# Performance work log

Hardware: AMD Instinct MI355X
Metric: run time of the kernel (lower is better)

## Reference

```python
import jax, jax.numpy as jnp
import numpy as np

E = 300   # embedding_dim
H = 300   # lstm hidden per direction
V = 200000
S = 128   # number of sentences
L = 128   # max sentence length
D = 2 * H # bilstm output dim == attention model_dim
NEG = -1e30


def setup_inputs() -> dict:
    key = jax.random.key(0)
    ks = jax.random.split(key, 12)
    sd = 0.05
    return {
        "tokens": jax.random.randint(ks[0], (S, L), 0, V, dtype=jnp.int32),
        "lengths": jax.random.randint(ks[1], (S,), 1, L + 1, dtype=jnp.int32),
        "table": jax.random.normal(ks[2], (V, E), jnp.float32) * sd,
        "Wih_f": jax.random.normal(ks[3], (4 * H, E), jnp.float32) * sd,
        "Whh_f": jax.random.normal(ks[4], (4 * H, H), jnp.float32) * sd,
        "bih_f": jax.random.normal(ks[5], (4 * H,), jnp.float32) * sd,
        "bhh_f": jax.random.normal(ks[6], (4 * H,), jnp.float32) * sd,
        "Wih_b": jax.random.normal(ks[7], (4 * H, E), jnp.float32) * sd,
        "Whh_b": jax.random.normal(ks[8], (4 * H, H), jnp.float32) * sd,
        "bih_b": jax.random.normal(ks[9], (4 * H,), jnp.float32) * sd,
        "bhh_b": jax.random.normal(ks[10], (4 * H,), jnp.float32) * sd,
    }


def _lstm_dir(x, Wih, Whh, bih, bhh, reverse):
    # x: [N, E] -> hs: [N, H]; PyTorch gate order (i, f, g, o)
    xw = x @ Wih.T + (bih + bhh)  # hoist input projection out of the scan

    def step(carry, xt):
        h, c = carry
        g = xt + h @ Whh.T
        i, f, gg, o = jnp.split(g, 4, axis=-1)
        c = jax.nn.sigmoid(f) * c + jax.nn.sigmoid(i) * jnp.tanh(gg)
        h = jax.nn.sigmoid(o) * jnp.tanh(c)
        return (h, c), h

    init = (jnp.zeros((H,), x.dtype), jnp.zeros((H,), x.dtype))
    _, hs = jax.lax.scan(step, init, xw, reverse=reverse)
    return hs


def reference(tokens, lengths, table, Wih_f, Whh_f, bih_f, bhh_f,
              Wih_b, Whh_b, bih_b, bhh_b):
    lens = np.asarray(lengths)                       # concrete lengths (static)
    rows = np.repeat(np.arange(S), lens)             # [N] sentence id per token
    cols = np.concatenate([np.arange(int(l)) for l in lens])  # [N] pos in sentence

    flat_ids = tokens[rows, cols]                    # ragged concat of all sentences, [N]
    embeds = table[flat_ids]                         # [N, E]

    # single BiLSTM pass over the whole concatenated token stream (batch=1)
    h_fwd = _lstm_dir(embeds, Wih_f, Whh_f, bih_f, bhh_f, reverse=False)
    h_bwd = _lstm_dir(embeds, Wih_b, Whh_b, bih_b, bhh_b, reverse=True)
    lstm_out = jnp.concatenate([h_fwd, h_bwd], axis=-1)  # [N, D]

    # scatter back to padded [S, L, D] so per-sentence attention is batched
    padded = jnp.zeros((S, L, D), lstm_out.dtype).at[rows, cols].set(lstm_out)
    mask = jnp.asarray(np.arange(L)[None, :] < lens[:, None])  # [S, L]

    # per-sentence scaled dot-product self-attention (Q=K=V=lstm_out slice)
    scores = jnp.einsum('sqd,skd->sqk', padded, padded) / jnp.sqrt(jnp.float32(D))
    scores = jnp.where(mask[:, None, :], scores, NEG)  # key padding mask
    attn = jax.nn.softmax(scores, axis=-1)
    ctx = jnp.einsum('sqk,skd->sqd', attn, padded)     # [S, L, D]

    # max-pool over valid positions of each sentence
    ctx = jnp.where(mask[:, :, None], ctx, NEG)
    return jnp.max(ctx, axis=1)                        # [S, D]
```

## Files before the change

kernel.cpp:

```cpp
#include <hip/hip_runtime.h>
#include <stdint.h>

#define S_ 128
#define L_ 128
#define E_ 300
#define H_ 300
#define NMAX (S_*L_)
#define R_ 1200
#define D_ 600
#define XW_STRIDE ((size_t)NMAX*R_)

__global__ void prep_kernel(const int* __restrict__ lengths, int* __restrict__ meta,
                            int* __restrict__ map, unsigned long long* __restrict__ hbuf) {
    __shared__ int offs[S_];
    int tid = threadIdx.x;
    if (tid == 0) {
        int acc = 0;
        for (int s = 0; s < S_; s++) { offs[s] = acc; acc += lengths[s]; }
        meta[0] = acc;
    }
    __syncthreads();
    for (int s = tid; s < S_; s += blockDim.x) {
        int o = offs[s], len = lengths[s];
        for (int l = 0; l < len; l++) map[o + l] = s * L_ + l;
    }
    for (int i = tid; i < 2*2*320; i += blockDim.x) hbuf[i] = 0ull;
}

__global__ __launch_bounds__(256, 1) void xw_kernel(
    const int* __restrict__ tokens, const float* __restrict__ table,
    const float* __restrict__ Wih_f, const float* __restrict__ bih_f, const float* __restrict__ bhh_f,
    const float* __restrict__ Wih_b, const float* __restrict__ bih_b, const float* __restrict__ bhh_b,
    const int* __restrict__ meta, const int* __restrict__ map, float* __restrict__ xw) {
    const int N = meta[0];
    const int n0 = blockIdx.x * 32;
    if (n0 >= N) return;
    const int r = blockIdx.y * 256 + threadIdx.x;
    const bool vr = (r < 2*R_);
    const int dir = (r >= R_) ? 1 : 0;
    const int rr = r - dir * R_;
    const float* W = dir ? Wih_b : Wih_f;
    float bias = 0.f;
    float4 w4[75];
    if (vr) {
        bias = dir ? (bih_b[rr] + bhh_b[rr]) : (bih_f[rr] + bhh_f[rr]);
        #pragma unroll
        for (int j = 0; j < 75; j++) w4[j] = *(const float4*)(W + (size_t)rr * E_ + 4*j);
    } else {
        #pragma unroll
        for (int j = 0; j < 75; j++) w4[j] = make_float4(0.f, 0.f, 0.f, 0.f);
    }
    float* xwd = xw + (size_t)dir * XW_STRIDE;
    const int iend = min(32, N - n0);
    for (int i = 0; i < iend; i++) {
        const int n = n0 + i;
        const int tok = tokens[map[n]];
        const float* arow = table + (size_t)tok * E_;
        float a0 = bias, a1 = 0.f, a2 = 0.f, a3 = 0.f;
        #pragma unroll
        for (int j = 0; j < 75; j++) {
            float4 a4 = *(const float4*)(arow + 4*j);
            a0 = fmaf(w4[j].x, a4.x, a0);
            a1 = fmaf(w4[j].y, a4.y, a1);
            a2 = fmaf(w4[j].z, a4.z, a2);
            a3 = fmaf(w4[j].w, a4.w, a3);
        }
        if (vr) xwd[(size_t)n * R_ + rr] = (a0 + a1) + (a2 + a3);
    }
}

__device__ __forceinline__ float sel4(int m, float a, float b, float c, float d) {
    float r = a;
    r = (m == 1) ? b : r;
    r = (m == 2) ? c : r;
    r = (m == 3) ? d : r;
    return r;
}
__device__ __forceinline__ float sigm(float x) {
    return __builtin_amdgcn_rcpf(1.f + __expf(-x));
}
__device__ __forceinline__ float tanh_fast(float x) {
    return 1.f - 2.f * __builtin_amdgcn_rcpf(1.f + __expf(2.f * x));
}

__global__ __launch_bounds__(256, 1) void scan_kernel(
    const float* __restrict__ Whh_f, const float* __restrict__ Whh_b,
    const int* __restrict__ meta, const int* __restrict__ map,
    unsigned long long* __restrict__ hbuf, const float* __restrict__ xw,
    float* __restrict__ padded) {
    const int N = meta[0];
    const int b = blockIdx.x;
    const int dir = b / 10;
    const int blk = b % 10;
    const int tid = threadIdx.x;
    const int wave = tid >> 6;
    const int lane = tid & 63;
    const int pair = tid >> 1;
    const int half = tid & 1;
    const int gate = pair & 3;
    const int d = 30 * blk + (pair >> 2);
    const bool vd = (pair < 120);

    __shared__ float w_lds[120][300];
    __shared__ float hl[4][300];

    const float* Whh = dir ? Whh_b : Whh_f;
    for (int i = tid; i < 120 * 75; i += 256) {
        const int lr = i / 75;
        const int c4 = (i % 75) * 4;
        const int grow = (lr & 3) * H_ + blk * 30 + (lr >> 2);
        *(float4*)(&w_lds[lr][c4]) = *(const float4*)(Whh + (size_t)grow * H_ + c4);
    }
    __syncthreads();

    const int row = gate * H_ + (vd ? d : 0);
    const int cbase = half ? 152 : 0;
    const float* wrow = vd ? &w_lds[pair][cbase] : &w_lds[0][cbase];

    const float* xwd = xw + (size_t)dir * XW_STRIDE;
    unsigned long long* hb = hbuf + dir * 2 * 320;
    float* hw = hl[wave];

    float c = 0.f;
    const bool storer = (vd && gate == 0 && half == 0);
    const int pd = dir * H_ + d;

    for (int t = 0; t < N; t++) {
        const int n = dir ? (N - 1 - t) : t;
        const float xw_t = vd ? xwd[(size_t)n * R_ + row] : 0.f;
        const int   m_t  = map[n];

        const unsigned long long* hp = hb + (size_t)(t & 1) * 320;
        const unsigned int want = (unsigned int)t;
        unsigned long long v0, v1, v2, v3, v4;
        for (;;) {
            v0 = __hip_atomic_load(hp + lane,        __ATOMIC_RELAXED, __HIP_MEMORY_SCOPE_AGENT);
            v1 = __hip_atomic_load(hp + 64  + lane,  __ATOMIC_RELAXED, __HIP_MEMORY_SCOPE_AGENT);
            v2 = __hip_atomic_load(hp + 128 + lane,  __ATOMIC_RELAXED, __HIP_MEMORY_SCOPE_AGENT);
            v3 = __hip_atomic_load(hp + 192 + lane,  __ATOMIC_RELAXED, __HIP_MEMORY_SCOPE_AGENT);
            v4 = (lane < 44) ? __hip_atomic_load(hp + 256 + lane, __ATOMIC_RELAXED, __HIP_MEMORY_SCOPE_AGENT)
                             : ((unsigned long long)want << 32);
            bool ok = ((unsigned int)(v0 >> 32) == want) &&
                      ((unsigned int)(v1 >> 32) == want) &&
                      ((unsigned int)(v2 >> 32) == want) &&
                      ((unsigned int)(v3 >> 32) == want) &&
                      ((unsigned int)(v4 >> 32) == want);
            if (ok) break;
        }
        hw[lane]        = __uint_as_float((unsigned int)v0);
        hw[64  + lane]  = __uint_as_float((unsigned int)v1);
        hw[128 + lane]  = __uint_as_float((unsigned int)v2);
        hw[192 + lane]  = __uint_as_float((unsigned int)v3);
        if (lane < 44) hw[256 + lane] = __uint_as_float((unsigned int)v4);

        const float* hbase = hw + cbase;
        float a0 = 0.f, a1 = 0.f, a2 = 0.f, a3 = 0.f;
        #pragma unroll
        for (int j = 0; j < 37; j++) {
            const float4 wj = *(const float4*)(wrow + 4*j);
            const float4 h4 = *(const float4*)(hbase + 4*j);
            a0 = fmaf(wj.x, h4.x, a0);
            a1 = fmaf(wj.y, h4.y, a1);
            a2 = fmaf(wj.z, h4.z, a2);
            a3 = fmaf(wj.w, h4.w, a3);
        }
        if (half == 0) {
            const float4 wj = *(const float4*)(wrow + 148);
            const float4 h4 = *(const float4*)(hbase + 148);
            a0 = fmaf(wj.x, h4.x, a0);
            a1 = fmaf(wj.y, h4.y, a1);
            a2 = fmaf(wj.z, h4.z, a2);
            a3 = fmaf(wj.w, h4.w, a3);
        }
        float sum = (a0 + a1) + (a2 + a3);
        sum += __shfl_xor(sum, 1);
        const float acc = xw_t + sum;

        const float aa = acc;
        const float bb = __shfl_xor(acc, 2);
        const float cc = __shfl_xor(acc, 4);
        const float dd = __shfl_xor(bb, 4);
        const float vi = sel4(gate,     aa, bb, cc, dd);
        const float vf = sel4(gate ^ 1, aa, bb, cc, dd);
        const float vg = sel4(gate ^ 2, aa, bb, cc, dd);
        const float vo = sel4(gate ^ 3, aa, bb, cc, dd);

        c = sigm(vf) * c + sigm(vi) * tanh_fast(vg);
        const float h = sigm(vo) * tanh_fast(c);

        if (storer) {
            const unsigned long long pv =
                ((unsigned long long)(unsigned int)(t + 1) << 32) |
                (unsigned long long)__float_as_uint(h);
            __hip_atomic_store(hb + (size_t)((t + 1) & 1) * 320 + d, pv,
                               __ATOMIC_RELAXED, __HIP_MEMORY_SCOPE_AGENT);
            padded[(size_t)m_t * D_ + pd] = h;
        }
    }
}

__global__ __launch_bounds__(256) void attn_kernel(
    const int* __restrict__ lengths, const float* __restrict__ padded,
    float* __restrict__ out) {
    const int s = blockIdx.x;
    const int tid = threadIdx.x;
    const int Ls = lengths[s];
    const float* P = padded + (size_t)s * L_ * D_;
    __shared__ float sc[16][128];
    const float scale = 0.040824829046386304f;
    float vmax0 = -1e30f, vmax1 = -1e30f, vmax2 = -1e30f;

    const int nqt = (Ls + 15) / 16;
    for (int qt = 0; qt < nqt; qt++) {
        const int q0 = qt * 16;
        if (tid < 128) {
            float acc[16];
            #pragma unroll
            for (int i = 0; i < 16; i++) acc[i] = -1e30f;
            if (tid < Ls) {
                #pragma unroll
                for (int i = 0; i < 16; i++) acc[i] = 0.f;
                const float* pk = P + (size_t)tid * D_;
                for (int e4 = 0; e4 < 150; e4++) {
                    const float4 k4 = *(const float4*)(pk + 4*e4);
                    #pragma unroll
                    for (int i = 0; i < 16; i++) {
                        const float4 q4 = *(const float4*)(P + (size_t)(q0 + i) * D_ + 4*e4);
                        acc[i] = fmaf(k4.x, q4.x, acc[i]);
                        acc[i] = fmaf(k4.y, q4.y, acc[i]);
                        acc[i] = fmaf(k4.z, q4.z, acc[i]);
                        acc[i] = fmaf(k4.w, q4.w, acc[i]);
                    }
                }
                #pragma unroll
                for (int i = 0; i < 16; i++) acc[i] *= scale;
            }
            #pragma unroll
            for (int i = 0; i < 16; i++) sc[i][tid] = acc[i];
        }
        __syncthreads();

        {
            const int w = tid >> 6, l = tid & 63;
            #pragma unroll
            for (int ii = 0; ii < 4; ii++) {
                const int i = w * 4 + ii;
                float x0 = sc[i][l], x1 = sc[i][64 + l];
                float mx = fmaxf(x0, x1);
                #pragma unroll
                for (int off = 32; off; off >>= 1) mx = fmaxf(mx, __shfl_xor(mx, off));
                float e0 = expf(x0 - mx), e1 = expf(x1 - mx);
                float sm = e0 + e1;
                #pragma unroll
                for (int off = 32; off; off >>= 1) sm += __shfl_xor(sm, off);
                const float inv = 1.f / sm;
                sc[i][l] = e0 * inv;
                sc[i][64 + l] = e1 * inv;
            }
        }
        __syncthreads();

        #pragma unroll
        for (int j = 0; j < 3; j++) {
            const int dd = j * 256 + tid;
            if (dd < D_) {
                float ca[16];
                #pragma unroll
                for (int i = 0; i < 16; i++) ca[i] = 0.f;
                for (int k4 = 0; k4 < 32; k4++) {
                    const float p0 = P[(size_t)(4*k4 + 0) * D_ + dd];
                    const float p1 = P[(size_t)(4*k4 + 1) * D_ + dd];
                    const float p2 = P[(size_t)(4*k4 + 2) * D_ + dd];
                    const float p3 = P[(size_t)(4*k4 + 3) * D_ + dd];
                    #pragma unroll
                    for (int i = 0; i < 16; i++) {
                        const float4 pr = *(const float4*)(&sc[i][4*k4]);
                        ca[i] = fmaf(pr.x, p0, ca[i]);
                        ca[i] = fmaf(pr.y, p1, ca[i]);
                        ca[i] = fmaf(pr.z, p2, ca[i]);
                        ca[i] = fmaf(pr.w, p3, ca[i]);
                    }
                }
                float vm = (j == 0) ? vmax0 : (j == 1) ? vmax1 : vmax2;
                #pragma unroll
                for (int i = 0; i < 16; i++)
                    if (q0 + i < Ls) vm = fmaxf(vm, ca[i]);
                if (j == 0) vmax0 = vm; else if (j == 1) vmax1 = vm; else vmax2 = vm;
            }
        }
        __syncthreads();
    }
    if (tid < D_)        out[(size_t)s * D_ + tid] = vmax0;
    if (256 + tid < D_)  out[(size_t)s * D_ + 256 + tid] = vmax1;
    if (512 + tid < D_)  out[(size_t)s * D_ + 512 + tid] = vmax2;
}

extern "C" void kernel_launch(void* const* d_in, const int* in_sizes, int n_in,
                              void* d_out, int out_size, void* d_ws, size_t ws_size,
                              hipStream_t stream) {
    const int*   tokens  = (const int*)d_in[0];
    const int*   lengths = (const int*)d_in[1];
    const float* table   = (const float*)d_in[2];
    const float* Wih_f   = (const float*)d_in[3];
    const float* Whh_f   = (const float*)d_in[4];
    const float* bih_f   = (const float*)d_in[5];
    const float* bhh_f   = (const float*)d_in[6];
    const float* Wih_b   = (const float*)d_in[7];
    const float* Whh_b   = (const float*)d_in[8];
    const float* bih_b   = (const float*)d_in[9];
    const float* bhh_b   = (const float*)d_in[10];
    float* out = (float*)d_out;

    char* ws = (char*)d_ws;
    int* meta                 = (int*)(ws + 0);
    int* map                  = (int*)(ws + 256);
    unsigned long long* hbuf  = (unsigned long long*)(ws + 256 + 65536);
    float* xw                 = (float*)(ws + 256 + 65536 + 10240);
    float* padded             = (float*)(ws + 256 + 65536 + 10240 + (size_t)2*NMAX*R_*4);

    prep_kernel<<<1, 256, 0, stream>>>(lengths, meta, map, hbuf);
    xw_kernel<<<dim3(NMAX/32, 10), 256, 0, stream>>>(tokens, table,
        Wih_f, bih_f, bhh_f, Wih_b, bih_b, bhh_b, meta, map, xw);
    scan_kernel<<<20, 256, 0, stream>>>(Whh_f, Whh_b, meta, map, hbuf, xw, padded);
    attn_kernel<<<S_, 256, 0, stream>>>(lengths, padded, out);
}
```

Before: 22.36 ms.

## Split input projection across four lanes, pad LDS weights, prefetch next xw

The input-projection kernel now splits each output row's dot product across four lanes, each holding a quarter of the weights, and combines them with shuffles. This cuts register pressure from 75 float4 to 19 and quadruples the grid. The recurrent scan pads the LDS weight rows to stride 305 with zeroed tails so both halves run a uniform 38-iteration loop. It also prefetches the next step's xw value and map entry before the matvec, hiding global load latency on the serial critical path. The costs are extra shuffles and redundant activation loads in the projection, and zero-padding work in the scan.

```diff
diff --git a/kernel.cpp b/kernel.cpp
--- a/kernel.cpp
+++ b/kernel.cpp
@@ -35,37 +35,50 @@
     const int N = meta[0];
     const int n0 = blockIdx.x * 32;
     if (n0 >= N) return;
-    const int r = blockIdx.y * 256 + threadIdx.x;
+    const int u = blockIdx.y * 256 + threadIdx.x;
+    const int r = u >> 2;
+    const int q = u & 3;
     const bool vr = (r < 2*R_);
     const int dir = (r >= R_) ? 1 : 0;
-    const int rr = r - dir * R_;
+    const int rr = vr ? (r - dir * R_) : 0;
     const float* W = dir ? Wih_b : Wih_f;
     float bias = 0.f;
-    float4 w4[75];
-    if (vr) {
-        bias = dir ? (bih_b[rr] + bhh_b[rr]) : (bih_f[rr] + bhh_f[rr]);
+    float4 w4[19];
+    {
+        const float* wr = W + (size_t)rr * E_ + q * 76;
         #pragma unroll
-        for (int j = 0; j < 75; j++) w4[j] = *(const float4*)(W + (size_t)rr * E_ + 4*j);
-    } else {
-        #pragma unroll
-        for (int j = 0; j < 75; j++) w4[j] = make_float4(0.f, 0.f, 0.f, 0.f);
-    }
+        for (int j = 0; j < 18; j++) w4[j] = vr ? *(const float4*)(wr + 4*j)
+                                                : make_float4(0.f,0.f,0.f,0.f);
+        w4[18] = (vr && q < 3) ? *(const float4*)(wr + 72) : make_float4(0.f,0.f,0.f,0.f);
+        if (vr && q == 0) bias = dir ? (bih_b[rr] + bhh_b[rr]) : (bih_f[rr] + bhh_f[rr]);
+    }
+    const int off18 = (q < 3) ? 72 : 0;
     float* xwd = xw + (size_t)dir * XW_STRIDE;
     const int iend = min(32, N - n0);
     for (int i = 0; i < iend; i++) {
         const int n = n0 + i;
         const int tok = tokens[map[n]];
-        const float* arow = table + (size_t)tok * E_;
+        const float* arow = table + (size_t)tok * E_ + q * 76;
         float a0 = bias, a1 = 0.f, a2 = 0.f, a3 = 0.f;
         #pragma unroll
-        for (int j = 0; j < 75; j++) {
+        for (int j = 0; j < 18; j++) {
             float4 a4 = *(const float4*)(arow + 4*j);
             a0 = fmaf(w4[j].x, a4.x, a0);
             a1 = fmaf(w4[j].y, a4.y, a1);
             a2 = fmaf(w4[j].z, a4.z, a2);
             a3 = fmaf(w4[j].w, a4.w, a3);
         }
-        if (vr) xwd[(size_t)n * R_ + rr] = (a0 + a1) + (a2 + a3);
+        {
+            float4 a4 = *(const float4*)(arow + off18);
+            a0 = fmaf(w4[18].x, a4.x, a0);
+            a1 = fmaf(w4[18].y, a4.y, a1);
+            a2 = fmaf(w4[18].z, a4.z, a2);
+            a3 = fmaf(w4[18].w, a4.w, a3);
+        }
+        float sum = (a0 + a1) + (a2 + a3);
+        sum += __shfl_xor(sum, 1);
+        sum += __shfl_xor(sum, 2);
+        if (vr && q == 0) xwd[(size_t)n * R_ + rr] = sum;
     }
 }
 
@@ -82,6 +95,8 @@
 __device__ __forceinline__ float tanh_fast(float x) {
     return 1.f - 2.f * __builtin_amdgcn_rcpf(1.f + __expf(2.f * x));
 }
+
+#define WSTRIDE 305
 
 __global__ __launch_bounds__(256, 1) void scan_kernel(
     const float* __restrict__ Whh_f, const float* __restrict__ Whh_b,
@@ -101,21 +116,24 @@
     const int d = 30 * blk + (pair >> 2);
     const bool vd = (pair < 120);
 
-    __shared__ float w_lds[120][300];
-    __shared__ float hl[4][300];
+    __shared__ float w_lds[120 * WSTRIDE];
+    __shared__ float hl[4][304];
 
     const float* Whh = dir ? Whh_b : Whh_f;
     for (int i = tid; i < 120 * 75; i += 256) {
-        const int lr = i / 75;
+        const int r2 = i / 75;
         const int c4 = (i % 75) * 4;
-        const int grow = (lr & 3) * H_ + blk * 30 + (lr >> 2);
-        *(float4*)(&w_lds[lr][c4]) = *(const float4*)(Whh + (size_t)grow * H_ + c4);
-    }
+        const int grow = (r2 & 3) * H_ + blk * 30 + (r2 >> 2);
+        *(float4*)(&w_lds[r2 * WSTRIDE + c4]) = *(const float4*)(Whh + (size_t)grow * H_ + c4);
+    }
+    for (int i = tid; i < 120 * 5; i += 256)
+        w_lds[(i / 5) * WSTRIDE + 300 + (i % 5)] = 0.f;
+    if (lane < 4) hl[wave][300 + lane] = 0.f;
     __syncthreads();
 
     const int row = gate * H_ + (vd ? d : 0);
-    const int cbase = half ? 152 : 0;
-    const float* wrow = vd ? &w_lds[pair][cbase] : &w_lds[0][cbase];
+    const int cbase = half * 152;
+    const float* wrow = &w_lds[(vd ? pair : 0) * WSTRIDE + cbase];
 
     const float* xwd = xw + (size_t)dir * XW_STRIDE;
     unsigned long long* hb = hbuf + dir * 2 * 320;
@@ -125,11 +143,11 @@
     const bool storer = (vd && gate == 0 && half == 0);
     const int pd = dir * H_ + d;
 
+    int n_cur = dir ? (N - 1) : 0;
+    float xw_cur = xwd[(size_t)n_cur * R_ + row];
+    int   m_cur  = map[n_cur];
+
     for (int t = 0; t < N; t++) {
-        const int n = dir ? (N - 1 - t) : t;
-        const float xw_t = vd ? xwd[(size_t)n * R_ + row] : 0.f;
-        const int   m_t  = map[n];
-
         const unsigned long long* hp = hb + (size_t)(t & 1) * 320;
         const unsigned int want = (unsigned int)t;
         unsigned long long v0, v1, v2, v3, v4;
@@ -153,10 +171,17 @@
         hw[192 + lane]  = __uint_as_float((unsigned int)v3);
         if (lane < 44) hw[256 + lane] = __uint_as_float((unsigned int)v4);
 
+        float xw_nxt = xw_cur; int m_nxt = m_cur;
+        if (t + 1 < N) {
+            const int nn = dir ? (N - 2 - t) : (t + 1);
+            xw_nxt = xwd[(size_t)nn * R_ + row];
+            m_nxt  = map[nn];
+        }
+
         const float* hbase = hw + cbase;
         float a0 = 0.f, a1 = 0.f, a2 = 0.f, a3 = 0.f;
         #pragma unroll
-        for (int j = 0; j < 37; j++) {
+        for (int j = 0; j < 38; j++) {
             const float4 wj = *(const float4*)(wrow + 4*j);
             const float4 h4 = *(const float4*)(hbase + 4*j);
             a0 = fmaf(wj.x, h4.x, a0);
@@ -164,17 +189,9 @@
             a2 = fmaf(wj.z, h4.z, a2);
             a3 = fmaf(wj.w, h4.w, a3);
         }
-        if (half == 0) {
-            const float4 wj = *(const float4*)(wrow + 148);
-            const float4 h4 = *(const float4*)(hbase + 148);
-            a0 = fmaf(wj.x, h4.x, a0);
-            a1 = fmaf(wj.y, h4.y, a1);
-            a2 = fmaf(wj.z, h4.z, a2);
-            a3 = fmaf(wj.w, h4.w, a3);
-        }
         float sum = (a0 + a1) + (a2 + a3);
         sum += __shfl_xor(sum, 1);
-        const float acc = xw_t + sum;
+        const float acc = xw_cur + sum;
 
         const float aa = acc;
         const float bb = __shfl_xor(acc, 2);
@@ -194,8 +211,10 @@
                 (unsigned long long)__float_as_uint(h);
             __hip_atomic_store(hb + (size_t)((t + 1) & 1) * 320 + d, pv,
                                __ATOMIC_RELAXED, __HIP_MEMORY_SCOPE_AGENT);
-            padded[(size_t)m_t * D_ + pd] = h;
-        }
+            padded[(size_t)m_cur * D_ + pd] = h;
+        }
+        xw_cur = xw_nxt;
+        m_cur  = m_nxt;
     }
 }
 
@@ -319,7 +338,7 @@
     float* padded             = (float*)(ws + 256 + 65536 + 10240 + (size_t)2*NMAX*R_*4);
 
     prep_kernel<<<1, 256, 0, stream>>>(lengths, meta, map, hbuf);
-    xw_kernel<<<dim3(NMAX/32, 10), 256, 0, stream>>>(tokens, table,
+    xw_kernel<<<dim3(NMAX/32, 40), 256, 0, stream>>>(tokens, table,
         Wih_f, bih_f, bhh_f, Wih_b, bih_b, bhh_b, meta, map, xw);
     scan_kernel<<<20, 256, 0, stream>>>(Whh_f, Whh_b, meta, map, hbuf, xw, padded);
     attn_kernel<<<S_, 256, 0, stream>>>(lengths, padded, out);
```

After: 46.74 ms. 109% more time.
